# Kernel optimization log

Measured on AMD Instinct MI355X. Metric: run time of the kernel, lower is better.

The kernel has to match this reference:

```python
import jax, jax.numpy as jnp
import numpy as np

B, C, H, W = 16, 256, 96, 96
K = 3
K2 = K * K


def setup_inputs() -> dict:
    key = jax.random.key(0)
    ks = jax.random.split(key, 8)
    s = 1.0 / np.sqrt(C)  # fan-in style scale for 1x1 convs
    sk = 1.0 / np.sqrt(K2)
    return {
        "x": jax.random.normal(ks[0], (B, C, H, W), jnp.float32),
        "w_xproj": jax.random.normal(ks[1], (C, C), jnp.float32) * s,
        "b_xproj": jnp.zeros((C,), jnp.float32),
        "w_proj": jax.random.normal(ks[2], (C, C), jnp.float32) * s,
        "b_proj": jnp.zeros((C,), jnp.float32),
        "w_kp": jax.random.normal(ks[3], (C, C), jnp.float32) * s,
        "b_kp": jnp.zeros((C,), jnp.float32),
        "w_kg": jax.random.normal(ks[4], (K2, K2), jnp.float32) * sk,
        "b_kg": jnp.zeros((K2,), jnp.float32),
        "diff_ctrl": jnp.zeros((1, 1, 1, C), jnp.float32),
    }


def reference(x, w_xproj, b_xproj, w_proj, b_proj, w_kp, b_kp, w_kg, b_kg, diff_ctrl):
    b, c, h, w = x.shape
    # --- kernel synthesis ---
    # 1x1 conv (kernel_proj)
    kp = jnp.einsum('bchw,oc->bohw', x, w_kp) + b_kp[None, :, None, None]
    # AdaptiveAvgPool1d over flattened spatial dim -> 9 bins (H*W divisible by 9)
    pooled = kp.reshape(b, c, K2, (h * w) // K2).mean(axis=-1)  # [B, C, 9]
    pooled = jax.nn.gelu(pooled)
    # per-channel Linear(9 -> 9): y = W @ v + b
    ker = jnp.einsum('bck,jk->bcj', pooled, w_kg) + b_kg  # [B, C, 9]
    # rearrange 'c (k1 k2) -> k1 k2 1 c' (batched)
    ker = ker.reshape(b, c, K, K).transpose(0, 2, 3, 1)[:, :, :, None, :]  # [B, K, K, 1, C]
    # lateral inhibition: subtract learned fraction of per-channel kernel mean
    factor = jax.nn.sigmoid(diff_ctrl)  # [1, 1, 1, C]
    ker = ker - factor * ker.mean(axis=(1, 2, 3), keepdims=True)
    # --- main path ---
    xp = jnp.einsum('bchw,oc->bohw', x, w_xproj) + b_xproj[None, :, None, None]
    pad = K // 2

    def dwconv(xi, ki):  # xi [C,H,W], ki [K,K,1,C]
        return jax.lax.conv_general_dilated(
            xi[None], ki, window_strides=(1, 1),
            padding=((pad, pad), (pad, pad)),
            dimension_numbers=('NCHW', 'HWIO', 'NCHW'),
            feature_group_count=c)[0]

    y = jax.vmap(dwconv)(xp, ker)  # per-sample dynamic depthwise conv
    out = jnp.einsum('bchw,oc->bohw', y, w_proj) + b_proj[None, :, None, None]
    return out
```

## Files before the change

### kernel.cpp

```cpp
#include <hip/hip_runtime.h>
#include <hip/hip_bf16.h>

#define CCH 256
#define HWP 9216
#define IMGDIM 96

typedef __attribute__((ext_vector_type(8))) short s16x8;
typedef __attribute__((ext_vector_type(4))) float f32x4;

__device__ __forceinline__ unsigned short f2bf(float f){
  __hip_bfloat16 h = __float2bfloat16(f);
  return *reinterpret_cast<unsigned short*>(&h);
}
__device__ __forceinline__ float bf2f(unsigned short h){
  return __uint_as_float(((unsigned)h) << 16);
}

__global__ void k0_convert(const float* __restrict__ wx, const float* __restrict__ wp,
                           unsigned short* __restrict__ wxb, unsigned short* __restrict__ wpb){
  int i = blockIdx.x * 256 + threadIdx.x;
  wxb[i] = f2bf(wx[i]);
  wpb[i] = f2bf(wp[i]);
}

__device__ __forceinline__ void gemm_chunk(const unsigned short* __restrict__ wbf,
                                           const unsigned short* buf,
                                           f32x4 acc[4][4], int lane, int obase, int c0){
  const int g = lane >> 4, r = lane & 15;
  #pragma unroll
  for (int kk = 0; kk < 2; ++kk){
    const int kc = kk*32 + g*8;
    s16x8 afr[4], bfr[4];
    #pragma unroll
    for (int nf = 0; nf < 4; ++nf){
      const int p = nf*16 + r;
      unsigned off = (unsigned)(p*128 + kc*2) ^ ((unsigned)(p & 7) << 4);
      bfr[nf] = *(const s16x8*)((const char*)buf + off);
    }
    #pragma unroll
    for (int mf = 0; mf < 4; ++mf)
      afr[mf] = *(const s16x8*)(wbf + (size_t)(obase + mf*16 + r)*CCH + c0 + kc);
    #pragma unroll
    for (int mf = 0; mf < 4; ++mf){
      #pragma unroll
      for (int nf = 0; nf < 4; ++nf){
        acc[mf][nf] = __builtin_amdgcn_mfma_f32_16x16x32_bf16(afr[mf], bfr[nf], acc[mf][nf], 0, 0, 0);
      }
    }
  }
}

__device__ __forceinline__ void k1_load(const float* __restrict__ xb, int p0, int c0,
                                        int pg, int cgl, float v[4][4]){
  #pragma unroll
  for (int ci = 0; ci < 4; ++ci){
    float4 q = *(const float4*)(xb + (size_t)(c0 + cgl*4 + ci)*HWP + p0 + pg*4);
    v[ci][0]=q.x; v[ci][1]=q.y; v[ci][2]=q.z; v[ci][3]=q.w;
  }
}
__device__ __forceinline__ void k1_store(unsigned short* buf, int pg, int cgl, float v[4][4],
                                         float* __restrict__ xpart, int c0, int lane, int bbase){
  #pragma unroll
  for (int pj = 0; pj < 4; ++pj){
    const int p = pg*4 + pj;
    unsigned off = (unsigned)(p*128 + cgl*8) ^ ((unsigned)(p & 7) << 4);
    ushort4 pk;
    pk.x = f2bf(v[0][pj]); pk.y = f2bf(v[1][pj]);
    pk.z = f2bf(v[2][pj]); pk.w = f2bf(v[3][pj]);
    *(ushort4*)((char*)buf + off) = pk;
  }
  #pragma unroll
  for (int ci = 0; ci < 4; ++ci){
    float s = v[ci][0] + v[ci][1] + v[ci][2] + v[ci][3];
    s += __shfl_xor(s, 1); s += __shfl_xor(s, 2);
    s += __shfl_xor(s, 4); s += __shfl_xor(s, 8);
    if ((lane & 15) == 0) xpart[bbase + c0 + cgl*4 + ci] = s;
  }
}

__global__ __launch_bounds__(256) void k1_xproj(const float* __restrict__ x,
    const unsigned short* __restrict__ wxb, const float* __restrict__ bx,
    unsigned short* __restrict__ xp, float* __restrict__ xpart){
  const int tile = blockIdx.x, b = blockIdx.y;
  const int p0 = tile * 64;
  const int t = threadIdx.x, lane = t & 63, wave = t >> 6;
  __shared__ __align__(16) unsigned short xlds[2][64*64];

  const float* xb = x + (size_t)b * CCH * HWP;
  const int binj = p0 >> 10, blk = (p0 >> 6) & 15;
  const int bbase = (((int)b*9 + binj)*16 + blk)*CCH;
  const int pg = t & 15, cgl = t >> 4;

  float v[2][4][4];
  f32x4 acc[4][4];
  f32x4 zz = {0.f,0.f,0.f,0.f};
  #pragma unroll
  for (int i2=0;i2<4;++i2){
    #pragma unroll
    for (int j2=0;j2<4;++j2) acc[i2][j2] = zz;
  }

  k1_load(xb, p0, 0, pg, cgl, v[0]);
  k1_store(xlds[0], pg, cgl, v[0], xpart, 0, lane, bbase);

  #pragma unroll
  for (int ch = 0; ch < 4; ++ch){
    __syncthreads();
    if (ch < 3) k1_load(xb, p0, (ch+1)*64, pg, cgl, v[(ch+1)&1]);
    gemm_chunk(wxb, xlds[ch & 1], acc, lane, wave*64, ch*64);
    if (ch < 3) k1_store(xlds[(ch+1)&1], pg, cgl, v[(ch+1)&1], xpart, (ch+1)*64, lane, bbase);
  }

  unsigned short* eb = &xlds[0][0];
  const int g = lane >> 4, r = lane & 15;
  #pragma unroll
  for (int h = 0; h < 2; ++h){
    __syncthreads();
    if ((wave >> 1) == h){
      const int mw = wave & 1;
      #pragma unroll
      for (int mf = 0; mf < 4; ++mf){
        const int o  = mw*64 + mf*16 + 4*g;
        const int og = h*128 + o;
        float b0 = bx[og], b1 = bx[og+1], b2 = bx[og+2], b3 = bx[og+3];
        #pragma unroll
        for (int nf = 0; nf < 4; ++nf){
          const int p = nf*16 + r;
          unsigned off = (unsigned)(p*256 + o*2) ^ ((unsigned)(p & 7) << 4);
          ushort4 pk;
          pk.x = f2bf(acc[mf][nf][0] + b0);
          pk.y = f2bf(acc[mf][nf][1] + b1);
          pk.z = f2bf(acc[mf][nf][2] + b2);
          pk.w = f2bf(acc[mf][nf][3] + b3);
          *(ushort4*)((char*)eb + off) = pk;
        }
      }
    }
    __syncthreads();
    const size_t gb = ((size_t)b*HWP + p0)*CCH + h*128;
    #pragma unroll
    for (int it = 0; it < 4; ++it){
      const unsigned u = it*256 + t;
      const unsigned p = u >> 4, unit = u & 15;
      const unsigned srcoff = (u*16u) ^ ((p & 7) << 4);
      uint4 val = *(const uint4*)((const char*)eb + srcoff);
      *(uint4*)(xp + gb + (size_t)p*CCH + unit*8) = val;
    }
  }
}

__global__ __launch_bounds__(256) void k2a_pooled(const float* __restrict__ xpart,
    const float* __restrict__ wkp, const float* __restrict__ bkp,
    float* __restrict__ pooledg){
  const int j = blockIdx.x, b = blockIdx.y, t = threadIdx.x;
  __shared__ float xbar[256];
  __shared__ float wch[256][65];
  const float* xp0 = xpart + (((size_t)b*9 + j)*16)*CCH;
  float s = 0.f;
  #pragma unroll
  for (int blk = 0; blk < 16; ++blk) s += xp0[blk*CCH + t];
  xbar[t] = s * (1.0f/1024.0f);
  float acc = bkp[t];
  for (int ch = 0; ch < 4; ++ch){
    __syncthreads();
    for (int u = t; u < 256*64; u += 256){
      wch[u >> 6][u & 63] = wkp[(size_t)(u >> 6)*CCH + ch*64 + (u & 63)];
    }
    __syncthreads();
    #pragma unroll
    for (int c = 0; c < 64; ++c) acc += wch[t][c] * xbar[ch*64 + c];
  }
  float x3 = acc*acc*acc;
  float tg = tanhf(0.7978845608028654f*(acc + 0.044715f*x3));
  pooledg[((size_t)b*9 + j)*CCH + t] = 0.5f*acc*(1.0f + tg);
}

__global__ void k2b_ker(const float* __restrict__ pooledg, const float* __restrict__ wkg,
                        const float* __restrict__ bkg, const float* __restrict__ dctrl,
                        float* __restrict__ kerg){
  const int b = blockIdx.x, c = threadIdx.x;
  float pl[9];
  #pragma unroll
  for (int k = 0; k < 9; ++k) pl[k] = pooledg[((size_t)b*9 + k)*CCH + c];
  float kv[9]; float m = 0.f;
  #pragma unroll
  for (int jp = 0; jp < 9; ++jp){
    float s2 = bkg[jp];
    #pragma unroll
    for (int k = 0; k < 9; ++k) s2 += pl[k] * wkg[jp*9 + k];
    kv[jp] = s2; m += s2;
  }
  m *= (1.0f/9.0f);
  float f = 1.0f / (1.0f + expf(-dctrl[c]));
  #pragma unroll
  for (int jp = 0; jp < 9; ++jp) kerg[((size_t)b*9 + jp)*CCH + c] = kv[jp] - f*m;
}

__global__ __launch_bounds__(256, 3) void k3i_conv(const unsigned short* __restrict__ xp,
    const unsigned short* __restrict__ wpb, const float* __restrict__ bp,
    const float* __restrict__ kerg, float* __restrict__ out){
  const int tile = blockIdx.x, b = blockIdx.y;
  const int th0 = (tile / 3) * 2, tw0 = (tile % 3) * 32;
  const int t = threadIdx.x, lane = t & 63, wave = t >> 6;
  __shared__ __align__(16) unsigned short halo[136*64];
  __shared__ __align__(16) unsigned short ylds[2][64*64];
  __shared__ __align__(16) float kl[9][256];

  for (int u = t; u < 9*256; u += 256)
    kl[u >> 8][u & 255] = kerg[((size_t)b*9 + (u >> 8))*CCH + (u & 255)];

  const unsigned short* xpb = xp + (size_t)b * HWP * CCH;
  const int p = t >> 2, dh = p >> 5, dw = p & 31, q = t & 3;

  uint4 sreg[5];
  f32x4 acc[4][4];
  f32x4 zz = {0.f,0.f,0.f,0.f};
  #pragma unroll
  for (int i2=0;i2<4;++i2){
    #pragma unroll
    for (int j2=0;j2<4;++j2) acc[i2][j2] = zz;
  }

  #define K3I_ISSUE(CH)                                                        \
    _Pragma("unroll")                                                          \
    for (int i = 0; i < 5; ++i){                                               \
      const int u = i*256 + t;                                                 \
      if (u < 1088){                                                           \
        const int pos = u >> 3, w8 = u & 7;                                    \
        const int rr = pos / 34, cc = pos % 34;                                \
        const int hh = th0 + rr - 1, ww = tw0 + cc - 1;                        \
        uint4 val = {0u,0u,0u,0u};                                             \
        if (hh >= 0 && hh < IMGDIM && ww >= 0 && ww < IMGDIM)                  \
          val = *(const uint4*)(xpb + ((size_t)(hh*IMGDIM + ww))*CCH + (CH)*64 + w8*8); \
        sreg[i] = val;                                                         \
      }                                                                        \
    }
  #define K3I_WRITE()                                                         \
    _Pragma("unroll")                                                          \
    for (int i = 0; i < 5; ++i){                                               \
      const int u = i*256 + t;                                                 \
      if (u < 1088){                                                           \
        const int pos = u >> 3, w8 = u & 7;                                    \
        unsigned off = (unsigned)(pos*128 + w8*16) ^ ((unsigned)(pos & 7) << 4); \
        *(uint4*)((char*)halo + off) = sreg[i];                                \
      }                                                                        \
    }
  #define K3I_CONV(CH)                                                        \
    _Pragma("unroll")                                                          \
    for (int ci = 0; ci < 2; ++ci){                                            \
      const int c = q*16 + ci*8;                                               \
      const int cg = (CH)*64 + c;                                              \
      float a8[8] = {0,0,0,0,0,0,0,0};                                         \
      _Pragma("unroll")                                                        \
      for (int tap = 0; tap < 9; ++tap){                                       \
        const int pos = (dh + tap/3)*34 + (dw + tap%3);                        \
        unsigned hof = (unsigned)(pos*128 + c*2) ^ ((unsigned)(pos & 7) << 4); \
        union { uint4 qv; unsigned short u16[8]; } hv;                         \
        hv.qv = *(const uint4*)((const char*)halo + hof);                      \
        const float4* kp4 = (const float4*)&kl[tap][cg];                       \
        float4 ka = kp4[0], kb = kp4[1];                                       \
        a8[0] += bf2f(hv.u16[0]) * ka.x;                                       \
        a8[1] += bf2f(hv.u16[1]) * ka.y;                                       \
        a8[2] += bf2f(hv.u16[2]) * ka.z;                                       \
        a8[3] += bf2f(hv.u16[3]) * ka.w;                                       \
        a8[4] += bf2f(hv.u16[4]) * kb.x;                                       \
        a8[5] += bf2f(hv.u16[5]) * kb.y;                                       \
        a8[6] += bf2f(hv.u16[6]) * kb.z;                                       \
        a8[7] += bf2f(hv.u16[7]) * kb.w;                                       \
      }                                                                        \
      unsigned pk[4];                                                          \
      _Pragma("unroll")                                                        \
      for (int e = 0; e < 4; ++e)                                              \
        pk[e] = (unsigned)f2bf(a8[2*e]) | ((unsigned)f2bf(a8[2*e+1]) << 16);   \
      unsigned yoff = (unsigned)(p*128 + c*2) ^ ((unsigned)(p & 7) << 4);      \
      *(uint4*)((char*)ylds[(CH) & 1] + yoff) = *(uint4*)pk;                   \
    }

  K3I_ISSUE(0)
  K3I_WRITE()
  __syncthreads();
  K3I_CONV(0)
  __syncthreads();

  #pragma unroll
  for (int ch = 1; ch < 4; ++ch){
    K3I_ISSUE(ch)
    gemm_chunk(wpb, ylds[(ch-1)&1], acc, lane, wave*64, (ch-1)*64);
    K3I_WRITE()
    __syncthreads();
    K3I_CONV(ch)
    __syncthreads();
  }
  #undef K3I_ISSUE
  #undef K3I_WRITE
  #undef K3I_CONV

  gemm_chunk(wpb, ylds[1], acc, lane, wave*64, 192);

  const int g = lane >> 4, r = lane & 15;
  #pragma unroll
  for (int mf = 0; mf < 4; ++mf){
    const int o = wave*64 + mf*16 + 4*g;
    float b0 = bp[o], b1 = bp[o+1], b2 = bp[o+2], b3 = bp[o+3];
    #pragma unroll
    for (int nf = 0; nf < 4; ++nf){
      const size_t pix = (size_t)(th0 + (nf >> 1))*IMGDIM + tw0 + (nf & 1)*16 + r;
      out[((size_t)b*CCH + o + 0)*HWP + pix] = acc[mf][nf][0] + b0;
      out[((size_t)b*CCH + o + 1)*HWP + pix] = acc[mf][nf][1] + b1;
      out[((size_t)b*CCH + o + 2)*HWP + pix] = acc[mf][nf][2] + b2;
      out[((size_t)b*CCH + o + 3)*HWP + pix] = acc[mf][nf][3] + b3;
    }
  }
}

extern "C" void kernel_launch(void* const* d_in, const int* in_sizes, int n_in,
                              void* d_out, int out_size, void* d_ws, size_t ws_size,
                              hipStream_t stream){
  const float* x   = (const float*)d_in[0];
  const float* wxp = (const float*)d_in[1];
  const float* bxp = (const float*)d_in[2];
  const float* wpr = (const float*)d_in[3];
  const float* bpr = (const float*)d_in[4];
  const float* wkp = (const float*)d_in[5];
  const float* bkp = (const float*)d_in[6];
  const float* wkg = (const float*)d_in[7];
  const float* bkg = (const float*)d_in[8];
  const float* dct = (const float*)d_in[9];

  char* ws = (char*)d_ws;
  unsigned short* wxb   = (unsigned short*)(ws + 0);
  unsigned short* wpb   = (unsigned short*)(ws + 131072);
  float*          xpart = (float*)(ws + 262144);
  float*          pooled= (float*)(ws + 2621440);
  float*          kerg  = (float*)(ws + 2768896);
  unsigned short* xp    = (unsigned short*)(ws + 2916352);
  float* o = (float*)d_out;

  k0_convert<<<256, 256, 0, stream>>>(wxp, wpr, wxb, wpb);
  k1_xproj<<<dim3(144,16), 256, 0, stream>>>(x, wxb, bxp, xp, xpart);
  k2a_pooled<<<dim3(9,16), 256, 0, stream>>>(xpart, wkp, bkp, pooled);
  k2b_ker<<<16, 256, 0, stream>>>(pooled, wkg, bkg, dct, kerg);
  k3i_conv<<<dim3(144,16), 256, 0, stream>>>(xp, wpb, bpr, kerg, o);
}
```

Measured before the change: 259.1 us.

## Warp-specialize conv kernel into producer and MFMA consumer waves

Splits the fused depthwise-conv plus projection kernel into 512-thread blocks: four producer waves load halos and compute the depthwise conv into double-buffered LDS, while four consumer waves run the MFMA projection GEMM on the previous chunk. The halo buffer is now double-buffered so the next chunk's load overlaps the current conv. The goal is to overlap the VALU conv with the matrix GEMM instead of running them serially in the same waves. The cost is more LDS per block and larger blocks, which may cut occupancy, and each wave group now idles while the other finishes.

```diff
diff --git a/kernel.cpp b/kernel.cpp
--- a/kernel.cpp
+++ b/kernel.cpp
@@ -196,21 +196,25 @@
   for (int jp = 0; jp < 9; ++jp) kerg[((size_t)b*9 + jp)*CCH + c] = kv[jp] - f*m;
 }
 
-__global__ __launch_bounds__(256, 3) void k3i_conv(const unsigned short* __restrict__ xp,
+__global__ __launch_bounds__(512, 4) void k3w_conv(const unsigned short* __restrict__ xp,
     const unsigned short* __restrict__ wpb, const float* __restrict__ bp,
     const float* __restrict__ kerg, float* __restrict__ out){
   const int tile = blockIdx.x, b = blockIdx.y;
   const int th0 = (tile / 3) * 2, tw0 = (tile % 3) * 32;
-  const int t = threadIdx.x, lane = t & 63, wave = t >> 6;
-  __shared__ __align__(16) unsigned short halo[136*64];
+  const int t = threadIdx.x, wave = t >> 6, lane = t & 63;
+  const bool prod = (wave < 4);
+  __shared__ __align__(16) unsigned short halo[2][136*64];
   __shared__ __align__(16) unsigned short ylds[2][64*64];
   __shared__ __align__(16) float kl[9][256];
 
-  for (int u = t; u < 9*256; u += 256)
-    kl[u >> 8][u & 255] = kerg[((size_t)b*9 + (u >> 8))*CCH + (u & 255)];
+  if (prod){
+    for (int u = t; u < 9*256; u += 256)
+      kl[u >> 8][u & 255] = kerg[((size_t)b*9 + (u >> 8))*CCH + (u & 255)];
+  }
 
   const unsigned short* xpb = xp + (size_t)b * HWP * CCH;
-  const int p = t >> 2, dh = p >> 5, dw = p & 31, q = t & 3;
+  const int p = (t & 255) >> 2, dh = p >> 5, dw = p & 31, q = t & 3;
+  const int obase = (wave - 4) * 64;
 
   uint4 sreg[5];
   f32x4 acc[4][4];
@@ -221,7 +225,7 @@
     for (int j2=0;j2<4;++j2) acc[i2][j2] = zz;
   }
 
-  #define K3I_ISSUE(CH)                                                        \
+  #define K3W_ISSUE(CH)                                                        \
     _Pragma("unroll")                                                          \
     for (int i = 0; i < 5; ++i){                                               \
       const int u = i*256 + t;                                                 \
@@ -235,17 +239,17 @@
         sreg[i] = val;                                                         \
       }                                                                        \
     }
-  #define K3I_WRITE()                                                         \
+  #define K3W_WRITE(BUF)                                                      \
     _Pragma("unroll")                                                          \
     for (int i = 0; i < 5; ++i){                                               \
       const int u = i*256 + t;                                                 \
       if (u < 1088){                                                           \
         const int pos = u >> 3, w8 = u & 7;                                    \
         unsigned off = (unsigned)(pos*128 + w8*16) ^ ((unsigned)(pos & 7) << 4); \
-        *(uint4*)((char*)halo + off) = sreg[i];                                \
+        *(uint4*)((char*)halo[BUF] + off) = sreg[i];                           \
       }                                                                        \
     }
-  #define K3I_CONV(CH)                                                        \
+  #define K3W_CONV(CH)                                                        \
     _Pragma("unroll")                                                          \
     for (int ci = 0; ci < 2; ++ci){                                            \
       const int c = q*16 + ci*8;                                               \
@@ -256,7 +260,7 @@
         const int pos = (dh + tap/3)*34 + (dw + tap%3);                        \
         unsigned hof = (unsigned)(pos*128 + c*2) ^ ((unsigned)(pos & 7) << 4); \
         union { uint4 qv; unsigned short u16[8]; } hv;                         \
-        hv.qv = *(const uint4*)((const char*)halo + hof);                      \
+        hv.qv = *(const uint4*)((const char*)halo[(CH) & 1] + hof);            \
         const float4* kp4 = (const float4*)&kl[tap][cg];                       \
         float4 ka = kp4[0], kb = kp4[1];                                       \
         a8[0] += bf2f(hv.u16[0]) * ka.x;                                       \
@@ -276,39 +280,43 @@
       *(uint4*)((char*)ylds[(CH) & 1] + yoff) = *(uint4*)pk;                   \
     }
 
-  K3I_ISSUE(0)
-  K3I_WRITE()
+  if (prod){
+    K3W_ISSUE(0)
+    K3W_WRITE(0)
+  }
   __syncthreads();
-  K3I_CONV(0)
-  __syncthreads();
-
-  #pragma unroll
-  for (int ch = 1; ch < 4; ++ch){
-    K3I_ISSUE(ch)
-    gemm_chunk(wpb, ylds[(ch-1)&1], acc, lane, wave*64, (ch-1)*64);
-    K3I_WRITE()
-    __syncthreads();
-    K3I_CONV(ch)
-    __syncthreads();
-  }
-  #undef K3I_ISSUE
-  #undef K3I_WRITE
-  #undef K3I_CONV
-
-  gemm_chunk(wpb, ylds[1], acc, lane, wave*64, 192);
-
-  const int g = lane >> 4, r = lane & 15;
-  #pragma unroll
-  for (int mf = 0; mf < 4; ++mf){
-    const int o = wave*64 + mf*16 + 4*g;
-    float b0 = bp[o], b1 = bp[o+1], b2 = bp[o+2], b3 = bp[o+3];
-    #pragma unroll
-    for (int nf = 0; nf < 4; ++nf){
-      const size_t pix = (size_t)(th0 + (nf >> 1))*IMGDIM + tw0 + (nf & 1)*16 + r;
-      out[((size_t)b*CCH + o + 0)*HWP + pix] = acc[mf][nf][0] + b0;
-      out[((size_t)b*CCH + o + 1)*HWP + pix] = acc[mf][nf][1] + b1;
-      out[((size_t)b*CCH + o + 2)*HWP + pix] = acc[mf][nf][2] + b2;
-      out[((size_t)b*CCH + o + 3)*HWP + pix] = acc[mf][nf][3] + b3;
+
+  #pragma unroll
+  for (int ch = 0; ch < 4; ++ch){
+    if (prod){
+      if (ch < 3) K3W_ISSUE(ch+1)
+      K3W_CONV(ch)
+      if (ch < 3) K3W_WRITE((ch+1)&1)
+    } else {
+      if (ch > 0) gemm_chunk(wpb, ylds[(ch-1)&1], acc, lane, obase, (ch-1)*64);
+    }
+    __syncthreads();
+  }
+  #undef K3W_ISSUE
+  #undef K3W_WRITE
+  #undef K3W_CONV
+
+  if (!prod){
+    gemm_chunk(wpb, ylds[1], acc, lane, obase, 192);
+
+    const int g = lane >> 4, r = lane & 15;
+    #pragma unroll
+    for (int mf = 0; mf < 4; ++mf){
+      const int o = obase + mf*16 + 4*g;
+      float b0 = bp[o], b1 = bp[o+1], b2 = bp[o+2], b3 = bp[o+3];
+      #pragma unroll
+      for (int nf = 0; nf < 4; ++nf){
+        const size_t pix = (size_t)(th0 + (nf >> 1))*IMGDIM + tw0 + (nf & 1)*16 + r;
+        out[((size_t)b*CCH + o + 0)*HWP + pix] = acc[mf][nf][0] + b0;
+        out[((size_t)b*CCH + o + 1)*HWP + pix] = acc[mf][nf][1] + b1;
+        out[((size_t)b*CCH + o + 2)*HWP + pix] = acc[mf][nf][2] + b2;
+        out[((size_t)b*CCH + o + 3)*HWP + pix] = acc[mf][nf][3] + b3;
+      }
     }
   }
 }
@@ -340,5 +348,5 @@
   k1_xproj<<<dim3(144,16), 256, 0, stream>>>(x, wxb, bxp, xp, xpart);
   k2a_pooled<<<dim3(9,16), 256, 0, stream>>>(xpart, wkp, bkp, pooled);
   k2b_ker<<<16, 256, 0, stream>>>(pooled, wkg, bkg, dct, kerg);
-  k3i_conv<<<dim3(144,16), 256, 0, stream>>>(xp, wpb, bpr, kerg, o);
-}
+  k3w_conv<<<dim3(144,16), 512, 0, stream>>>(xp, wpb, bpr, kerg, o);
+}
```

Measured after the change: 349.7 us. 1.35x slower.
